# Performance work log

Measured on AMD Instinct MI355X. Metric: run time of the kernel, lower is better.

The kernel has to match this reference:

```python
import jax, jax.numpy as jnp
import numpy as np

CONF_THRESHOLD = 0.25
IOU_THRESHOLD = 0.5
MAX_OUT_DETS = 300
CELL_DIM = 640.0
PRE_NMS_TOPK = 4096  # fixed-size candidate set for jit-compatible NMS
N_ANCHORS = 134400   # 2560px input, strides 8/16/32
N_CLASSES = 80


def setup_inputs() -> dict:
    key = jax.random.key(0)
    preds = jax.random.uniform(key, (1, 4 + N_CLASSES, N_ANCHORS), dtype=jnp.float32)
    # scale the 4 box channels (xc, yc, w, h) to pixel range, keep class scores in [0,1]
    scale = jnp.concatenate([jnp.full((4,), CELL_DIM, jnp.float32),
                             jnp.ones((N_CLASSES,), jnp.float32)])
    preds = preds * scale[None, :, None]
    return {"yolo_preds": preds}


def _pairwise_iou(boxes):
    # boxes: [K, 4] in x1,y1,x2,y2 — torchvision-style IoU (no +1)
    area = (boxes[:, 2] - boxes[:, 0]) * (boxes[:, 3] - boxes[:, 1])
    lt = jnp.maximum(boxes[:, None, :2], boxes[None, :, :2])
    rb = jnp.minimum(boxes[:, None, 2:], boxes[None, :, 2:])
    wh = jnp.clip(rb - lt, 0.0)
    inter = wh[..., 0] * wh[..., 1]
    union = area[:, None] + area[None, :] - inter
    return inter / (union + 1e-9)


def _forward(yolo_preds):
    p = yolo_preds[0]                      # [4+C, A] (batch index [0] as in original)
    cls = p[4:4 + N_CLASSES]               # [C, A]
    scores = jnp.max(cls, axis=0)          # [A]
    classes = jnp.argmax(cls, axis=0)      # [A] int

    # box decode: note torch float `//` is floor division
    xc, yc, w, h = p[0], p[1], p[2], p[3]
    hw = jnp.floor(w / 2.0)
    hh = jnp.floor(h / 2.0)
    boxes = jnp.stack([xc - hw, yc - hh, xc + hw, yc + hh], axis=1)  # [A, 4]

    # confidence threshold mask (jit-compatible: mask to -inf instead of dynamic filter)
    masked = jnp.where(scores >= CONF_THRESHOLD, scores, -jnp.inf)

    # fixed-size pre-NMS top-k candidate selection (sorted descending)
    cand_scores, idx = jax.lax.top_k(masked, PRE_NMS_TOPK)   # [K]
    cand_boxes = boxes[idx]                                   # [K, 4]
    cand_classes = classes[idx]                               # [K]
    cand_valid = jnp.isfinite(cand_scores)                    # padding / below-threshold

    # greedy class-agnostic NMS (original uses plain torchvision.ops.nms)
    iou = _pairwise_iou(cand_boxes)                           # [K, K]
    k_idx = jnp.arange(PRE_NMS_TOPK)
    suppress = (iou > IOU_THRESHOLD) & (k_idx[None, :] > k_idx[:, None])  # j>i upper tri

    def body(i, keep):
        sup = suppress[i] & keep[i]
        return keep & ~sup

    keep = jax.lax.fori_loop(0, PRE_NMS_TOPK, body, cand_valid)

    # final top-k among survivors
    kept_scores = jnp.where(keep, cand_scores, -jnp.inf)
    final_scores, fidx = jax.lax.top_k(kept_scores, MAX_OUT_DETS)
    final_valid = jnp.isfinite(final_scores)
    final_boxes = jnp.where(final_valid[:, None], cand_boxes[fidx] / CELL_DIM, 0.0)
    final_classes = jnp.where(final_valid, cand_classes[fidx], 0)
    final_scores = jnp.where(final_valid, final_scores, 0.0)

    # tie-break quirk from the original: if the last two scores are ~equal,
    # zero out every score within 1e-5 of the last one
    tie = jnp.abs(final_scores[-1] - final_scores[-2]) < 1e-6
    factor = jnp.where(tie,
                       (final_scores - final_scores[-1] > 1e-5).astype(final_scores.dtype),
                       jnp.ones((), final_scores.dtype))
    final_scores = final_scores * factor

    count = jnp.sum(final_scores > 1e-5)
    return final_boxes, final_scores, final_classes, count


def reference(yolo_preds):
    return _forward(yolo_preds)
```

## Files before the change

### kernel.cpp

```cpp
#include <hip/hip_runtime.h>
#include <math.h>

#define N_ANCH 134400
#define N_CLS  80
#define TOPK   4096
#define MAX_OUT 300
#define TIECAP 16384

#define SARR_OFF   0u
#define GHIST_OFF  537600u
#define STATE_OFF  541696u
#define CNT_OFF    541704u
#define TIECNT_OFF 541708u
#define ISTAR_OFF  541712u
#define TIEBUF_OFF 541728u
#define CANDK_OFF  607264u
#define CBOX_OFF   640032u
#define CSCORE_OFF 705568u
#define CCLS_OFF   721952u
#define SUP_OFF    738336u
#define WS_NEEDED  2835488u
#define MEMSET_OFF 537600u
#define MEMSET_LEN 4112u

static __device__ __forceinline__ unsigned int ord_f32(float f) {
  unsigned int u = __float_as_uint(f);
  return (u & 0x80000000u) ? ~u : (u | 0x80000000u);
}
static __device__ __forceinline__ float unord_f32(unsigned int o) {
  unsigned int u = (o & 0x80000000u) ? (o ^ 0x80000000u) : ~o;
  return __uint_as_float(u);
}

__global__ void k_keys(const float* __restrict__ p, unsigned int* __restrict__ sarr) {
  int i = blockIdx.x * blockDim.x + threadIdx.x;
  if (i >= N_ANCH) return;
  float best = p[4 * N_ANCH + i];
#pragma unroll 4
  for (int c = 1; c < N_CLS; ++c) {
    float v = p[(4 + c) * N_ANCH + i];
    best = fmaxf(best, v);
  }
  float m = (best >= 0.25f) ? best : -INFINITY;
  sarr[i] = ord_f32(m);
}

template <int PASS>
__global__ __launch_bounds__(256) void k_hist(const unsigned int* __restrict__ sarr,
                                              const unsigned int* __restrict__ state,
                                              unsigned int* __restrict__ ghist) {
  __shared__ unsigned int h[256];
  int tid = threadIdx.x;
  h[tid] = 0u;
  __syncthreads();
  int i = blockIdx.x * 256 + tid;
  unsigned int s = sarr[i];
  if (PASS == 0) {
    atomicAdd(&h[s >> 24], 1u);
  } else {
    const int sh = 24 - 8 * PASS;
    if ((s >> (sh + 8)) == state[0])
      atomicAdd(&h[(s >> sh) & 255u], 1u);
  }
  __syncthreads();
  if (h[tid]) atomicAdd(&ghist[PASS * 256 + tid], h[tid]);
}

template <int PASS>
__global__ __launch_bounds__(256) void k_scan(const unsigned int* __restrict__ ghist,
                                              unsigned int* __restrict__ state) {
  __shared__ unsigned int h[256];
  int tid = threadIdx.x;
  h[tid] = ghist[PASS * 256 + tid];
  __syncthreads();
  if (tid == 0) {
    unsigned int r    = (PASS == 0) ? (unsigned)TOPK : state[1];
    unsigned int pref = (PASS == 0) ? 0u : state[0];
    unsigned int cum = 0u;
    for (int b = 255; b >= 0; --b) {
      unsigned int c = h[b];
      if (cum + c >= r) { state[0] = (pref << 8) | (unsigned int)b; state[1] = r - cum; break; }
      cum += c;
    }
  }
}

__global__ void k_tiecollect(const unsigned int* __restrict__ sarr,
                             const unsigned int* __restrict__ state,
                             unsigned int* __restrict__ tiecnt,
                             unsigned int* __restrict__ tiebuf) {
  int i = blockIdx.x * 256 + threadIdx.x;
  if (sarr[i] == state[0]) {
    unsigned int pos = atomicAdd(tiecnt, 1u);
    if (pos < TIECAP) tiebuf[pos] = (unsigned int)i;
  }
}

__global__ __launch_bounds__(256) void k_tiesel(const unsigned int* __restrict__ state,
                                                const unsigned int* __restrict__ tiecnt,
                                                const unsigned int* __restrict__ tiebuf,
                                                unsigned int* __restrict__ Istar) {
  __shared__ unsigned int buf[TIECAP];
  unsigned int n = *tiecnt; if (n > TIECAP) n = TIECAP;
  unsigned int rf = state[1];
  for (unsigned int t = threadIdx.x; t < n; t += 256) buf[t] = tiebuf[t];
  __syncthreads();
  for (unsigned int t = threadIdx.x; t < n; t += 256) {
    unsigned int v = buf[t], r = 0u;
    for (unsigned int j = 0; j < n; ++j) r += (buf[j] < v) ? 1u : 0u;
    if (r == rf - 1u) *Istar = v;
  }
}

__global__ void k_gather(const unsigned int* __restrict__ sarr,
                         const unsigned int* __restrict__ state,
                         const unsigned int* __restrict__ Istar,
                         unsigned int* __restrict__ counter,
                         unsigned long long* __restrict__ candk) {
  int i = blockIdx.x * 256 + threadIdx.x;
  unsigned int s = sarr[i];
  unsigned int S = state[0];
  bool take = (s > S) || (s == S && (unsigned int)i <= *Istar);
  if (take) {
    unsigned int pos = atomicAdd(counter, 1u);
    if (pos < TOPK)
      candk[pos] = ((unsigned long long)s << 32) |
                   (unsigned long long)(~(unsigned int)i);
  }
}

__global__ __launch_bounds__(1024) void k_sort(unsigned long long* __restrict__ candk) {
  __shared__ unsigned long long s[TOPK];
  for (int i = threadIdx.x; i < TOPK; i += 1024) s[i] = candk[i];
  __syncthreads();
  for (int k = 2; k <= TOPK; k <<= 1) {
    for (int j = k >> 1; j > 0; j >>= 1) {
      for (int i = threadIdx.x; i < TOPK; i += 1024) {
        int ixj = i ^ j;
        if (ixj > i) {
          bool up = ((i & k) == 0);
          unsigned long long a = s[i], b = s[ixj];
          bool sw = up ? (a < b) : (a > b);
          if (sw) { s[i] = b; s[ixj] = a; }
        }
      }
      __syncthreads();
    }
  }
  for (int i = threadIdx.x; i < TOPK; i += 1024) candk[i] = s[i];
}

__global__ void k_fill(const float* __restrict__ p,
                       const unsigned long long* __restrict__ candk,
                       float4* __restrict__ cbox,
                       float* __restrict__ cscore,
                       int* __restrict__ ccls) {
  int c = blockIdx.x * blockDim.x + threadIdx.x;
  if (c >= TOPK) return;
  unsigned long long k = candk[c];
  float score = unord_f32((unsigned int)(k >> 32));
  int idx = (int)(~(unsigned int)(k & 0xFFFFFFFFull));
  float xc = p[idx];
  float yc = p[N_ANCH + idx];
  float w  = p[2 * N_ANCH + idx];
  float h  = p[3 * N_ANCH + idx];
  float hw = floorf(w * 0.5f), hh = floorf(h * 0.5f);
  cbox[c] = make_float4(xc - hw, yc - hh, xc + hw, yc + hh);
  float best = p[4 * N_ANCH + idx];
  int cls = 0;
  for (int cc = 1; cc < N_CLS; ++cc) {
    float v = p[(4 + cc) * N_ANCH + idx];
    if (v > best) { best = v; cls = cc; }
  }
  cscore[c] = score;
  ccls[c]   = cls;
}

__global__ void k_iou(const float4* __restrict__ cbox, unsigned long long* __restrict__ sup) {
  int g = blockIdx.x * blockDim.x + threadIdx.x;
  int row = g >> 6, word = g & 63;
  float4 bi = cbox[row];
  float ai = (bi.z - bi.x) * (bi.w - bi.y);
  unsigned long long m = 0ull;
  int j0 = word << 6;
  if (j0 + 63 > row) {
    for (int b = 0; b < 64; ++b) {
      int j = j0 + b;
      if (j <= row) continue;
      float4 bj = cbox[j];
      float aj = (bj.z - bj.x) * (bj.w - bj.y);
      float ltx = fmaxf(bi.x, bj.x), lty = fmaxf(bi.y, bj.y);
      float rbx = fminf(bi.z, bj.z), rby = fminf(bi.w, bj.w);
      float ww = fmaxf(rbx - ltx, 0.0f), hh = fmaxf(rby - lty, 0.0f);
      float inter = ww * hh;
      float uni = ai + aj - inter;
      float iou = inter / (uni + 1e-9f);
      if (iou > 0.5f) m |= (1ull << b);
    }
  }
  sup[g] = m;
}

__global__ __launch_bounds__(256) void k_nms_out(const float4* __restrict__ cbox,
                                                 const float* __restrict__ cscore,
                                                 const int* __restrict__ ccls,
                                                 const unsigned long long* __restrict__ sup,
                                                 float* __restrict__ out) {
  __shared__ unsigned long long skeep[64];
  __shared__ int s_list[MAX_OUT];
  __shared__ float s_fs[MAX_OUT];
  __shared__ int s_K;
  __shared__ int s_n0;
  __shared__ int s_cnt;
  int tid = threadIdx.x;
  int lane = tid & 63, wave = tid >> 6;

  for (int r = 0; r < 16; ++r) {
    float sc = cscore[r * 256 + tid];
    unsigned long long m = __ballot(sc >= 0.25f);
    if (lane == 0) skeep[r * 4 + wave] = m;
  }
  if (tid == 0) { s_K = 0; s_n0 = 0; s_cnt = 0; }
  __syncthreads();

  for (int chunk = 0; chunk < 64; ++chunk) {
    unsigned long long cur0 = skeep[chunk];
    if (cur0 == 0ull) continue;
    if (wave == 0) {
      unsigned long long diag = sup[(chunk * 64 + lane) * 64 + chunk];
      unsigned long long cur = cur0;
      int n = s_K;
      if (lane == 0) s_n0 = n;
      while (cur) {
        int b = __builtin_ctzll(cur);
        if (lane == 0) s_list[n] = chunk * 64 + b;
        n++;
        if (n == MAX_OUT) break;
        unsigned long long mb = __shfl(diag, b);
        cur &= ~mb;
        cur = (b == 63) ? 0ull : (cur & (~0ull << (b + 1)));
      }
      if (lane == 0) s_K = n;
    }
    __syncthreads();
    int n0 = s_n0, n1 = s_K;
    if (n1 >= MAX_OUT) break;
    unsigned long long acc = 0ull;
    for (int k = n0 + wave; k < n1; k += 4)
      acc |= sup[(unsigned)s_list[k] * 64 + lane];
    if (acc) atomicAnd(&skeep[lane], ~acc);
    __syncthreads();
  }
  __syncthreads();

  int K = s_K;
  for (int r = tid; r < MAX_OUT; r += 256)
    s_fs[r] = (r < K) ? cscore[s_list[r]] : 0.0f;
  __syncthreads();

  float slast = s_fs[MAX_OUT - 1], sprev = s_fs[MAX_OUT - 2];
  bool tie = fabsf(slast - sprev) < 1e-6f;
  int local = 0;
  for (int r = tid; r < MAX_OUT; r += 256) {
    float fs = s_fs[r];
    float factor = tie ? ((fs - slast > 1e-5f) ? 1.0f : 0.0f) : 1.0f;
    float so = fs * factor;
    out[4 * MAX_OUT + r] = so;
    if (so > 1e-5f) local++;
    if (r < K) {
      int c = s_list[r];
      float4 b = cbox[c];
      out[4 * r + 0] = b.x / 640.0f;
      out[4 * r + 1] = b.y / 640.0f;
      out[4 * r + 2] = b.z / 640.0f;
      out[4 * r + 3] = b.w / 640.0f;
      out[5 * MAX_OUT + r] = (float)ccls[c];
    } else {
      out[4 * r + 0] = 0.0f; out[4 * r + 1] = 0.0f;
      out[4 * r + 2] = 0.0f; out[4 * r + 3] = 0.0f;
      out[5 * MAX_OUT + r] = 0.0f;
    }
  }
  if (local) atomicAdd(&s_cnt, local);
  __syncthreads();
  if (tid == 0) out[6 * MAX_OUT] = (float)s_cnt;
}

extern "C" void kernel_launch(void* const* d_in, const int* in_sizes, int n_in,
                              void* d_out, int out_size, void* d_ws, size_t ws_size,
                              hipStream_t stream) {
  const float* p = (const float*)d_in[0];
  float* out = (float*)d_out;
  char* ws = (char*)d_ws;

  if (ws_size < (size_t)WS_NEEDED) return;

  unsigned int* sarr   = (unsigned int*)(ws + SARR_OFF);
  unsigned int* ghist  = (unsigned int*)(ws + GHIST_OFF);
  unsigned int* state  = (unsigned int*)(ws + STATE_OFF);
  unsigned int* counter= (unsigned int*)(ws + CNT_OFF);
  unsigned int* tiecnt = (unsigned int*)(ws + TIECNT_OFF);
  unsigned int* Istar  = (unsigned int*)(ws + ISTAR_OFF);
  unsigned int* tiebuf = (unsigned int*)(ws + TIEBUF_OFF);
  unsigned long long* candk = (unsigned long long*)(ws + CANDK_OFF);
  float4* cbox              = (float4*)(ws + CBOX_OFF);
  float* cscore             = (float*)(ws + CSCORE_OFF);
  int* ccls                 = (int*)(ws + CCLS_OFF);
  unsigned long long* sup   = (unsigned long long*)(ws + SUP_OFF);

  const int NB = N_ANCH / 256;

  hipMemsetAsync(ws + MEMSET_OFF, 0, MEMSET_LEN, stream);
  k_keys<<<NB, 256, 0, stream>>>(p, sarr);
  k_hist<0><<<NB, 256, 0, stream>>>(sarr, state, ghist);
  k_scan<0><<<1, 256, 0, stream>>>(ghist, state);
  k_hist<1><<<NB, 256, 0, stream>>>(sarr, state, ghist);
  k_scan<1><<<1, 256, 0, stream>>>(ghist, state);
  k_hist<2><<<NB, 256, 0, stream>>>(sarr, state, ghist);
  k_scan<2><<<1, 256, 0, stream>>>(ghist, state);
  k_hist<3><<<NB, 256, 0, stream>>>(sarr, state, ghist);
  k_scan<3><<<1, 256, 0, stream>>>(ghist, state);
  k_tiecollect<<<NB, 256, 0, stream>>>(sarr, state, tiecnt, tiebuf);
  k_tiesel<<<1, 256, 0, stream>>>(state, tiecnt, tiebuf, Istar);
  k_gather<<<NB, 256, 0, stream>>>(sarr, state, Istar, counter, candk);
  k_sort<<<1, 1024, 0, stream>>>(candk);
  k_fill<<<TOPK / 256, 256, 0, stream>>>(p, candk, cbox, cscore, ccls);
  k_iou<<<(TOPK * 64) / 256, 256, 0, stream>>>(cbox, sup);
  k_nms_out<<<1, 256, 0, stream>>>(cbox, cscore, ccls, sup, out);
}
```

Before: 358.8 us.

## Fuse histogram and argmax into key pass, merge tie handling, preload NMS rows

The key kernel now computes the argmax class (stored as bytes) and the first radix histogram, so the separate pass-0 histogram launch and the 80-class rescan in the fill kernel go away. Tie collection and candidate gathering are merged into one pass, and a single-block kernel appends the ranked tie entries directly. This drops two full-array launches. The NMS loop now preloads each chunk's suppression rows into registers and masks them with the kept bitmask instead of making dependent loads through the kept list. The cost is more register pressure and 16 extra loads per chunk, even for rows that end up unused.

```diff
diff --git a/kernel.cpp b/kernel.cpp
--- a/kernel.cpp
+++ b/kernel.cpp
@@ -12,14 +12,14 @@
 #define STATE_OFF  541696u
 #define CNT_OFF    541704u
 #define TIECNT_OFF 541708u
-#define ISTAR_OFF  541712u
-#define TIEBUF_OFF 541728u
-#define CANDK_OFF  607264u
-#define CBOX_OFF   640032u
-#define CSCORE_OFF 705568u
-#define CCLS_OFF   721952u
-#define SUP_OFF    738336u
-#define WS_NEEDED  2835488u
+#define CLS8_OFF   541712u
+#define TIEBUF_OFF 676112u
+#define CANDK_OFF  741648u
+#define CBOX_OFF   774416u
+#define CSCORE_OFF 839952u
+#define CCLS_OFF   856336u
+#define SUP_OFF    872720u
+#define WS_NEEDED  2969872u
 #define MEMSET_OFF 537600u
 #define MEMSET_LEN 4112u
 
@@ -32,17 +32,28 @@
   return __uint_as_float(u);
 }
 
-__global__ void k_keys(const float* __restrict__ p, unsigned int* __restrict__ sarr) {
-  int i = blockIdx.x * blockDim.x + threadIdx.x;
-  if (i >= N_ANCH) return;
+__global__ __launch_bounds__(256) void k_keys(const float* __restrict__ p,
+                                              unsigned int* __restrict__ sarr,
+                                              unsigned char* __restrict__ cls8,
+                                              unsigned int* __restrict__ ghist) {
+  __shared__ unsigned int h[256];
+  int tid = threadIdx.x;
+  h[tid] = 0u;
+  __syncthreads();
+  int i = blockIdx.x * 256 + tid;
   float best = p[4 * N_ANCH + i];
-#pragma unroll 4
+  int cls = 0;
   for (int c = 1; c < N_CLS; ++c) {
     float v = p[(4 + c) * N_ANCH + i];
-    best = fmaxf(best, v);
+    if (v > best) { best = v; cls = c; }
   }
   float m = (best >= 0.25f) ? best : -INFINITY;
-  sarr[i] = ord_f32(m);
+  unsigned int s = ord_f32(m);
+  sarr[i] = s;
+  cls8[i] = (unsigned char)cls;
+  atomicAdd(&h[s >> 24], 1u);
+  __syncthreads();
+  if (h[tid]) atomicAdd(&ghist[tid], h[tid]);
 }
 
 template <int PASS>
@@ -55,13 +66,9 @@
   __syncthreads();
   int i = blockIdx.x * 256 + tid;
   unsigned int s = sarr[i];
-  if (PASS == 0) {
-    atomicAdd(&h[s >> 24], 1u);
-  } else {
-    const int sh = 24 - 8 * PASS;
-    if ((s >> (sh + 8)) == state[0])
-      atomicAdd(&h[(s >> sh) & 255u], 1u);
-  }
+  const int sh = 24 - 8 * PASS;
+  if ((s >> (sh + 8)) == state[0])
+    atomicAdd(&h[(s >> sh) & 255u], 1u);
   __syncthreads();
   if (h[tid]) atomicAdd(&ghist[PASS * 256 + tid], h[tid]);
 }
@@ -85,47 +92,42 @@
   }
 }
 
-__global__ void k_tiecollect(const unsigned int* __restrict__ sarr,
-                             const unsigned int* __restrict__ state,
-                             unsigned int* __restrict__ tiecnt,
-                             unsigned int* __restrict__ tiebuf) {
-  int i = blockIdx.x * 256 + threadIdx.x;
-  if (sarr[i] == state[0]) {
-    unsigned int pos = atomicAdd(tiecnt, 1u);
-    if (pos < TIECAP) tiebuf[pos] = (unsigned int)i;
-  }
-}
-
-__global__ __launch_bounds__(256) void k_tiesel(const unsigned int* __restrict__ state,
-                                                const unsigned int* __restrict__ tiecnt,
-                                                const unsigned int* __restrict__ tiebuf,
-                                                unsigned int* __restrict__ Istar) {
-  __shared__ unsigned int buf[TIECAP];
-  unsigned int n = *tiecnt; if (n > TIECAP) n = TIECAP;
-  unsigned int rf = state[1];
-  for (unsigned int t = threadIdx.x; t < n; t += 256) buf[t] = tiebuf[t];
-  __syncthreads();
-  for (unsigned int t = threadIdx.x; t < n; t += 256) {
-    unsigned int v = buf[t], r = 0u;
-    for (unsigned int j = 0; j < n; ++j) r += (buf[j] < v) ? 1u : 0u;
-    if (r == rf - 1u) *Istar = v;
-  }
-}
-
-__global__ void k_gather(const unsigned int* __restrict__ sarr,
-                         const unsigned int* __restrict__ state,
-                         const unsigned int* __restrict__ Istar,
-                         unsigned int* __restrict__ counter,
-                         unsigned long long* __restrict__ candk) {
+__global__ void k_gathertie(const unsigned int* __restrict__ sarr,
+                            const unsigned int* __restrict__ state,
+                            unsigned int* __restrict__ counter,
+                            unsigned int* __restrict__ tiecnt,
+                            unsigned int* __restrict__ tiebuf,
+                            unsigned long long* __restrict__ candk) {
   int i = blockIdx.x * 256 + threadIdx.x;
   unsigned int s = sarr[i];
   unsigned int S = state[0];
-  bool take = (s > S) || (s == S && (unsigned int)i <= *Istar);
-  if (take) {
+  if (s > S) {
     unsigned int pos = atomicAdd(counter, 1u);
     if (pos < TOPK)
       candk[pos] = ((unsigned long long)s << 32) |
                    (unsigned long long)(~(unsigned int)i);
+  } else if (s == S) {
+    unsigned int tp = atomicAdd(tiecnt, 1u);
+    if (tp < TIECAP) tiebuf[tp] = (unsigned int)i;
+  }
+}
+
+__global__ __launch_bounds__(256) void k_tieappend(const unsigned int* __restrict__ state,
+                                                   const unsigned int* __restrict__ counter,
+                                                   const unsigned int* __restrict__ tiecnt,
+                                                   const unsigned int* __restrict__ tiebuf,
+                                                   unsigned long long* __restrict__ candk) {
+  __shared__ unsigned int buf[TIECAP];
+  unsigned int n = *tiecnt; if (n > TIECAP) n = TIECAP;
+  unsigned int rf = state[1];
+  unsigned int cnt0 = *counter;
+  unsigned long long Shi = ((unsigned long long)state[0]) << 32;
+  for (unsigned int t = threadIdx.x; t < n; t += 256) buf[t] = tiebuf[t];
+  __syncthreads();
+  for (unsigned int t = threadIdx.x; t < n; t += 256) {
+    unsigned int v = buf[t], r = 0u;
+    for (unsigned int j = 0; j < n; ++j) r += (buf[j] < v) ? 1u : 0u;
+    if (r < rf) candk[cnt0 + r] = Shi | (unsigned long long)(~v);
   }
 }
 
@@ -151,6 +153,7 @@
 }
 
 __global__ void k_fill(const float* __restrict__ p,
+                       const unsigned char* __restrict__ cls8,
                        const unsigned long long* __restrict__ candk,
                        float4* __restrict__ cbox,
                        float* __restrict__ cscore,
@@ -166,14 +169,8 @@
   float h  = p[3 * N_ANCH + idx];
   float hw = floorf(w * 0.5f), hh = floorf(h * 0.5f);
   cbox[c] = make_float4(xc - hw, yc - hh, xc + hw, yc + hh);
-  float best = p[4 * N_ANCH + idx];
-  int cls = 0;
-  for (int cc = 1; cc < N_CLS; ++cc) {
-    float v = p[(4 + cc) * N_ANCH + idx];
-    if (v > best) { best = v; cls = cc; }
-  }
   cscore[c] = score;
-  ccls[c]   = cls;
+  ccls[c]   = (int)cls8[idx];
 }
 
 __global__ void k_iou(const float4* __restrict__ cbox, unsigned long long* __restrict__ sup) {
@@ -207,10 +204,10 @@
                                                  const unsigned long long* __restrict__ sup,
                                                  float* __restrict__ out) {
   __shared__ unsigned long long skeep[64];
+  __shared__ unsigned long long s_keptl;
   __shared__ int s_list[MAX_OUT];
   __shared__ float s_fs[MAX_OUT];
   __shared__ int s_K;
-  __shared__ int s_n0;
   __shared__ int s_cnt;
   int tid = threadIdx.x;
   int lane = tid & 63, wave = tid >> 6;
@@ -220,34 +217,42 @@
     unsigned long long m = __ballot(sc >= 0.25f);
     if (lane == 0) skeep[r * 4 + wave] = m;
   }
-  if (tid == 0) { s_K = 0; s_n0 = 0; s_cnt = 0; }
+  if (tid == 0) { s_K = 0; s_cnt = 0; }
   __syncthreads();
 
   for (int chunk = 0; chunk < 64; ++chunk) {
     unsigned long long cur0 = skeep[chunk];
     if (cur0 == 0ull) continue;
+    unsigned long long rowv[16];
+#pragma unroll
+    for (int t = 0; t < 16; ++t)
+      rowv[t] = sup[(unsigned)(chunk * 64 + wave * 16 + t) * 64 + lane];
     if (wave == 0) {
       unsigned long long diag = sup[(chunk * 64 + lane) * 64 + chunk];
       unsigned long long cur = cur0;
+      unsigned long long keptl = 0ull;
       int n = s_K;
-      if (lane == 0) s_n0 = n;
       while (cur) {
         int b = __builtin_ctzll(cur);
         if (lane == 0) s_list[n] = chunk * 64 + b;
         n++;
+        keptl |= (1ull << b);
         if (n == MAX_OUT) break;
         unsigned long long mb = __shfl(diag, b);
         cur &= ~mb;
         cur = (b == 63) ? 0ull : (cur & (~0ull << (b + 1)));
       }
-      if (lane == 0) s_K = n;
+      if (lane == 0) { s_K = n; s_keptl = keptl; }
     }
     __syncthreads();
-    int n0 = s_n0, n1 = s_K;
-    if (n1 >= MAX_OUT) break;
+    if (s_K >= MAX_OUT) break;
+    unsigned long long keptl = s_keptl;
     unsigned long long acc = 0ull;
-    for (int k = n0 + wave; k < n1; k += 4)
-      acc |= sup[(unsigned)s_list[k] * 64 + lane];
+#pragma unroll
+    for (int t = 0; t < 16; ++t) {
+      unsigned long long sel = 0ull - ((keptl >> (wave * 16 + t)) & 1ull);
+      acc |= rowv[t] & sel;
+    }
     if (acc) atomicAnd(&skeep[lane], ~acc);
     __syncthreads();
   }
@@ -295,13 +300,13 @@
 
   if (ws_size < (size_t)WS_NEEDED) return;
 
-  unsigned int* sarr   = (unsigned int*)(ws + SARR_OFF);
-  unsigned int* ghist  = (unsigned int*)(ws + GHIST_OFF);
-  unsigned int* state  = (unsigned int*)(ws + STATE_OFF);
-  unsigned int* counter= (unsigned int*)(ws + CNT_OFF);
-  unsigned int* tiecnt = (unsigned int*)(ws + TIECNT_OFF);
-  unsigned int* Istar  = (unsigned int*)(ws + ISTAR_OFF);
-  unsigned int* tiebuf = (unsigned int*)(ws + TIEBUF_OFF);
+  unsigned int* sarr    = (unsigned int*)(ws + SARR_OFF);
+  unsigned int* ghist   = (unsigned int*)(ws + GHIST_OFF);
+  unsigned int* state   = (unsigned int*)(ws + STATE_OFF);
+  unsigned int* counter = (unsigned int*)(ws + CNT_OFF);
+  unsigned int* tiecnt  = (unsigned int*)(ws + TIECNT_OFF);
+  unsigned char* cls8   = (unsigned char*)(ws + CLS8_OFF);
+  unsigned int* tiebuf  = (unsigned int*)(ws + TIEBUF_OFF);
   unsigned long long* candk = (unsigned long long*)(ws + CANDK_OFF);
   float4* cbox              = (float4*)(ws + CBOX_OFF);
   float* cscore             = (float*)(ws + CSCORE_OFF);
@@ -311,8 +316,7 @@
   const int NB = N_ANCH / 256;
 
   hipMemsetAsync(ws + MEMSET_OFF, 0, MEMSET_LEN, stream);
-  k_keys<<<NB, 256, 0, stream>>>(p, sarr);
-  k_hist<0><<<NB, 256, 0, stream>>>(sarr, state, ghist);
+  k_keys<<<NB, 256, 0, stream>>>(p, sarr, cls8, ghist);
   k_scan<0><<<1, 256, 0, stream>>>(ghist, state);
   k_hist<1><<<NB, 256, 0, stream>>>(sarr, state, ghist);
   k_scan<1><<<1, 256, 0, stream>>>(ghist, state);
@@ -320,11 +324,10 @@
   k_scan<2><<<1, 256, 0, stream>>>(ghist, state);
   k_hist<3><<<NB, 256, 0, stream>>>(sarr, state, ghist);
   k_scan<3><<<1, 256, 0, stream>>>(ghist, state);
-  k_tiecollect<<<NB, 256, 0, stream>>>(sarr, state, tiecnt, tiebuf);
-  k_tiesel<<<1, 256, 0, stream>>>(state, tiecnt, tiebuf, Istar);
-  k_gather<<<NB, 256, 0, stream>>>(sarr, state, Istar, counter, candk);
+  k_gathertie<<<NB, 256, 0, stream>>>(sarr, state, counter, tiecnt, tiebuf, candk);
+  k_tieappend<<<1, 256, 0, stream>>>(state, counter, tiecnt, tiebuf, candk);
   k_sort<<<1, 1024, 0, stream>>>(candk);
-  k_fill<<<TOPK / 256, 256, 0, stream>>>(p, candk, cbox, cscore, ccls);
+  k_fill<<<TOPK / 256, 256, 0, stream>>>(p, cls8, candk, cbox, cscore, ccls);
   k_iou<<<(TOPK * 64) / 256, 256, 0, stream>>>(cbox, sup);
   k_nms_out<<<1, 256, 0, stream>>>(cbox, cscore, ccls, sup, out);
 }
```

After: 310.2 us. 13.5% less time.
